# Kernel tuning notes

Measured on AMD Instinct MI355X. Metric: run time of the kernel, lower is better.

The kernel has to match this reference:

```python
import jax, jax.numpy as jnp
import numpy as np

FULL_SCALE = 128.0
R = 0.5
TOPK = 4


def setup_inputs() -> dict:
    key = jax.random.key(0)
    k0, k1, k2, k3, k4 = jax.random.split(key, 5)
    B, Na, Nb, D = 16, 2048, 2048, 512
    coords_a = jax.random.randint(k0, (B, Na, 3), 0, 128, dtype=jnp.int32)
    coords_b = jax.random.randint(k1, (B, Nb, 3), 0, 128, dtype=jnp.int32)
    feats_a = jax.random.normal(k2, (B, Na, D), jnp.float32)
    feats_b = jax.random.normal(k3, (B, Nb, D), jnp.float32)
    W = jax.random.normal(k4, (2 * D, D), jnp.float32) / np.sqrt(2 * D).astype(np.float32)
    bias = jnp.zeros((D,), jnp.float32)
    return {"feats_a": feats_a, "feats_b": feats_b, "W": W, "bias": bias,
            "coords_a": coords_a, "coords_b": coords_b}


def _pairwise_l2(ca, cb):
    # ca: [B,Na,3], cb: [B,Nb,3] -> [B,Na,Nb], scaled by full_scale
    x2 = jnp.sum(ca * ca, axis=-1)[:, :, None]
    y2 = jnp.sum(cb * cb, axis=-1)[:, None, :]
    sq = x2 + y2 - 2.0 * jnp.einsum('bnd,bmd->bnm', ca, cb)
    return jnp.sqrt(jnp.clip(sq, 0.0, None)) / FULL_SCALE


def reference(feats_a, feats_b, W, bias, coords_a, coords_b):
    ca = coords_a.astype(jnp.float32)
    cb = coords_b.astype(jnp.float32)
    dist = _pairwise_l2(ca, cb)                       # [B,Na,Nb]
    neg_top, idx = jax.lax.top_k(-dist, TOPK)         # smallest TOPK distances
    dist_w = R - jnp.clip(-neg_top, 0.0, R)           # [B,Na,k]
    # gather neighbor features: [B,Na,k,D]
    b_f = jnp.take_along_axis(feats_b[:, None, :, :], idx[:, :, :, None], axis=2)
    a_f = feats_a[:, :, None, :]                      # broadcast over k
    h = jnp.concatenate([b_f, a_f - b_f], axis=-1)    # [B,Na,k,2D]
    fused = jnp.sum(jax.nn.relu(h @ W + bias) * dist_w[..., None], axis=2)  # [B,Na,D]
    # ME.cat(a, tmp): concatenate features along channel dim
    return jnp.concatenate([feats_a, fused], axis=-1)  # [B,Na,2D]
```

## Files before the change

kernel.cpp:

```cpp
#include <hip/hip_runtime.h>
#include <hip/hip_bf16.h>
#include <cstdint>
#include <cstddef>

#define NA   2048
#define NB   2048
#define DD   512

typedef __attribute__((ext_vector_type(8))) short bf16x8;
typedef __attribute__((ext_vector_type(4))) float f32x4;
typedef unsigned short u16;
typedef unsigned int   u32;

__device__ __forceinline__ u16 f2b_hw(float f) {
    u32 w;
    asm("v_cvt_pk_bf16_f32 %0, %1, %2" : "=v"(w) : "v"(f), "v"(f));
    return (u16)w;
}
__device__ __forceinline__ float b2f(u16 h) {
    return __uint_as_float(((u32)h) << 16);
}
__device__ __forceinline__ u32 umin32(u32 a, u32 b) { return a < b ? a : b; }
__device__ __forceinline__ u32 umax32(u32 a, u32 b) { return a > b ? a : b; }
__device__ __forceinline__ u32 med3u(u32 a, u32 b, u32 c) {
    return umax32(umin32(a, b), umin32(umax32(a, b), c));
}
__device__ __forceinline__ bf16x8 cvt8(f32x4 v0, f32x4 v1) {
    u32 w0, w1, w2, w3;
    asm("v_cvt_pk_bf16_f32 %0, %1, %2" : "=v"(w0) : "v"(v0[0]), "v"(v0[1]));
    asm("v_cvt_pk_bf16_f32 %0, %1, %2" : "=v"(w1) : "v"(v0[2]), "v"(v0[3]));
    asm("v_cvt_pk_bf16_f32 %0, %1, %2" : "=v"(w2) : "v"(v1[0]), "v"(v1[1]));
    asm("v_cvt_pk_bf16_f32 %0, %1, %2" : "=v"(w3) : "v"(v1[2]), "v"(v1[3]));
    union { u32 u[4]; bf16x8 v; } cv;
    cv.u[0] = w0; cv.u[1] = w1; cv.u[2] = w2; cv.u[3] = w3;
    return cv.v;
}

#define GLDS16(gsrc, ldst)                                                  \
    __builtin_amdgcn_global_load_lds(                                       \
        (const __attribute__((address_space(1))) void*)(gsrc),              \
        (__attribute__((address_space(3))) void*)(ldst), 16, 0, 0)

__global__ __launch_bounds__(256) void prep_w(const float* __restrict__ W,
                                              u16* __restrict__ W2T,
                                              u16* __restrict__ WdT) {
    __shared__ float s2[64][65];
    __shared__ float sd[64][65];
    int kb = blockIdx.x * 64, nb = blockIdx.y * 64;
    int tid = threadIdx.x;
    int c = tid & 63, r0 = tid >> 6;
    #pragma unroll
    for (int p = 0; p < 16; ++p) {
        int r = p * 4 + r0;
        float w1 = W[(size_t)(kb + r) * DD + nb + c];
        float w2 = W[(size_t)(512 + kb + r) * DD + nb + c];
        s2[r][c] = w2;
        sd[r][c] = w1 - w2;
    }
    __syncthreads();
    #pragma unroll
    for (int p = 0; p < 16; ++p) {
        int n = p * 4 + r0;
        W2T[(size_t)(nb + n) * DD + kb + c] = f2b_hw(s2[c][n]);
        WdT[(size_t)(nb + n) * DD + kb + c] = f2b_hw(sd[c][n]);
    }
}

__global__ __launch_bounds__(512) void topk_kernel(const int* __restrict__ ca,
                                                   const int* __restrict__ cb,
                                                   int* __restrict__ idx_out,
                                                   float* __restrict__ w_out) {
    __shared__ u32 pcb[NB];
    __shared__ u32 part[3 * 128 * 4];
    int b = blockIdx.y;
    int tid = threadIdx.x;
    for (int p = tid; p < NB; p += 512) {
        const int* c = cb + ((size_t)b * NB + p) * 3;
        pcb[p] = (u32)c[0] | ((u32)c[1] << 8) | ((u32)c[2] << 16);
    }
    __syncthreads();

    int q = tid & 127, g = tid >> 7;
    int i = blockIdx.x * 128 + q;
    const int* ac = ca + ((size_t)b * NA + i) * 3;
    int ax = ac[0], ay = ac[1], az = ac[2];

    u32 k0 = ~0u, k1 = ~0u, k2 = ~0u, k3 = ~0u;
    int j0 = g * 512;
    #pragma unroll 8
    for (int jj = 0; jj < 512; ++jj) {
        int j = j0 + jj;
        u32 p = pcb[j];
        int dx = ax - (int)(p & 255u);
        int dy = ay - (int)((p >> 8) & 255u);
        int dz = az - (int)(p >> 16);
        u32 s = (u32)(__mul24(dx, dx) + __mul24(dy, dy) + __mul24(dz, dz));
        u32 key = (s << 11) | (u32)j;
        u32 nk0 = umin32(k0, key);
        u32 nk1 = med3u(key, k0, k1);
        u32 nk2 = med3u(key, k1, k2);
        u32 nk3 = med3u(key, k2, k3);
        k0 = nk0; k1 = nk1; k2 = nk2; k3 = nk3;
    }
    if (g) {
        u32* pp = &part[((g - 1) * 128 + q) * 4];
        pp[0] = k0; pp[1] = k1; pp[2] = k2; pp[3] = k3;
    }
    __syncthreads();
    if (g == 0) {
        #pragma unroll
        for (int L = 0; L < 3; ++L) {
            const u32* pp = &part[(L * 128 + q) * 4];
            #pragma unroll
            for (int t = 0; t < 4; ++t) {
                u32 key = pp[t];
                u32 nk0 = umin32(k0, key);
                u32 nk1 = med3u(key, k0, k1);
                u32 nk2 = med3u(key, k1, k2);
                u32 nk3 = med3u(key, k2, k3);
                k0 = nk0; k1 = nk1; k2 = nk2; k3 = nk3;
            }
        }
        size_t o = ((size_t)b * NA + i) * 4;
        u32 ks[4] = {k0, k1, k2, k3};
        #pragma unroll
        for (int t = 0; t < 4; ++t) {
            idx_out[o + t] = (int)(ks[t] & 2047u);
            float d = sqrtf((float)(ks[t] >> 11)) * (1.0f / 128.0f);
            w_out[o + t] = 0.5f - fminf(d, 0.5f);
        }
    }
}

__global__ __launch_bounds__(256, 1) void gemm_qp(
    const float* __restrict__ fa, const float* __restrict__ fb,
    const u16* __restrict__ W2T, const u16* __restrict__ WdT,
    u16* __restrict__ Pb, u16* __restrict__ Qb) {

    __shared__ __align__(16) char smem[65536];

    const int bid  = blockIdx.x;
    const int half = bid >> 9;
    const int idx  = bid & 511;
    const float* A  = half ? fa : fb;
    const u16*   BT = half ? W2T : WdT;
    u16*         C  = half ? Pb : Qb;

    const int tid  = threadIdx.x;
    const int lane = tid & 63;
    const int wave = tid >> 6;
    const int m0   = (idx >> 1) << 7;
    const int n0   = (idx & 1) << 8;
    const int l15  = lane & 15;
    const int fq   = lane >> 4;
    const int wr   = (wave >> 1) << 6;
    const int wc   = (wave & 1) << 7;

    int aflat[4]; const float* asp[4];
    #pragma unroll
    for (int i = 0; i < 4; ++i) {
        int flat = i * 256 + tid;
        int row = flat >> 3, pq = flat & 7;
        aflat[i] = flat;
        asp[i] = A + (size_t)(m0 + row) * DD + ((pq ^ (row & 7)) << 2);
    }
    int bflat[4]; const u16* bsp[4];
    #pragma unroll
    for (int i = 0; i < 4; ++i) {
        int flat = i * 256 + tid;
        int row = flat >> 2, pq = flat & 3;
        bflat[i] = flat;
        bsp[i] = BT + (size_t)(n0 + row) * DD + ((pq ^ ((row >> 1) & 3)) << 3);
    }

    int aoff[4][2], boff[8];
    #pragma unroll
    for (int mf = 0; mf < 4; ++mf) {
        int R = wr + mf * 16 + l15;
        aoff[mf][0] = R * 128 + (((2 * fq) ^ (R & 7)) << 4);
        aoff[mf][1] = R * 128 + (((2 * fq + 1) ^ (R & 7)) << 4);
    }
    #pragma unroll
    for (int nf = 0; nf < 8; ++nf) {
        int R = wc + nf * 16 + l15;
        boff[nf] = 16384 + R * 64 + ((fq ^ ((R >> 1) & 3)) << 4);
    }

    f32x4 acc[4][8];
    #pragma unroll
    for (int mf = 0; mf < 4; ++mf)
        #pragma unroll
        for (int nf = 0; nf < 8; ++nf)
            acc[mf][nf] = (f32x4){0.f, 0.f, 0.f, 0.f};

#define STAGE(kk, bufb)                                                      \
    { _Pragma("unroll") for (int i = 0; i < 4; ++i)                          \
          GLDS16(asp[i] + (kk), smem + (bufb) + aflat[i] * 16);              \
      _Pragma("unroll") for (int i = 0; i < 4; ++i)                          \
          GLDS16(bsp[i] + (kk), smem + (bufb) + 16384 + bflat[i] * 16); }

    STAGE(0, 0);

    #pragma unroll 1
    for (int t = 0; t < 16; ++t) {
        const int cur = (t & 1) * 32768;
        if (t < 15) {
            STAGE((t + 1) * 32, 32768 - cur);
            asm volatile("s_waitcnt vmcnt(8)" ::: "memory");
        } else {
            asm volatile("s_waitcnt vmcnt(0)" ::: "memory");
        }
        __builtin_amdgcn_s_barrier();

        bf16x8 af[4], bfr[8];
        #pragma unroll
        for (int mf = 0; mf < 4; ++mf) {
            f32x4 lo = *(const f32x4*)(smem + cur + aoff[mf][0]);
            f32x4 hi = *(const f32x4*)(smem + cur + aoff[mf][1]);
            af[mf] = cvt8(lo, hi);
        }
        #pragma unroll
        for (int nf = 0; nf < 8; ++nf)
            bfr[nf] = *(const bf16x8*)(smem + cur + boff[nf]);
        #pragma unroll
        for (int mf = 0; mf < 4; ++mf)
            #pragma unroll
            for (int nf = 0; nf < 8; ++nf)
                acc[mf][nf] = __builtin_amdgcn_mfma_f32_16x16x32_bf16(
                    af[mf], bfr[nf], acc[mf][nf], 0, 0, 0);

        __builtin_amdgcn_s_barrier();
    }

    const int r4 = (lane >> 4) * 4;
    #pragma unroll
    for (int mf = 0; mf < 4; ++mf)
        #pragma unroll
        for (int nf = 0; nf < 8; ++nf)
            #pragma unroll
            for (int j = 0; j < 4; ++j) {
                int row = m0 + wr + mf * 16 + r4 + j;
                int col = n0 + wc + nf * 16 + l15;
                C[(size_t)row * DD + col] = f2b_hw(acc[mf][nf][j]);
            }
}

__global__ __launch_bounds__(256) void epilogue_kernel(
    const float* __restrict__ fa, const u16* __restrict__ Pb,
    const u16* __restrict__ Qb, const int* __restrict__ idxb,
    const float* __restrict__ wb, const float* __restrict__ bias,
    float* __restrict__ out) {

    int bid = blockIdx.x;
    int ob  = (bid & 7) * 1024 + (bid >> 3);
    int tid  = threadIdx.x;
    int r    = ob * 4 + (tid >> 6);
    int lane = tid & 63;
    int c8   = lane * 8;
    int b    = r >> 11;

    const int*   ip = idxb + (size_t)r * 4;
    const float* wp = wb + (size_t)r * 4;
    int   i0 = ip[0], i1 = ip[1], i2 = ip[2], i3 = ip[3];
    float w0 = wp[0], w1 = wp[1], w2 = wp[2], w3 = wp[3];

    const float* ar = fa + (size_t)r * DD + c8;
    f32x4 a0 = *(const f32x4*)ar;
    f32x4 a1 = *(const f32x4*)(ar + 4);

    bf16x8 pv = *(const bf16x8*)(Pb + (size_t)r * DD + c8);
    f32x4 bia0 = *(const f32x4*)(bias + c8);
    f32x4 bia1 = *(const f32x4*)(bias + c8 + 4);

    size_t qbase = ((size_t)b << 11) * DD;
    bf16x8 qv0 = *(const bf16x8*)(Qb + qbase + (size_t)i0 * DD + c8);
    bf16x8 qv1 = *(const bf16x8*)(Qb + qbase + (size_t)i1 * DD + c8);
    bf16x8 qv2 = *(const bf16x8*)(Qb + qbase + (size_t)i2 * DD + c8);
    bf16x8 qv3 = *(const bf16x8*)(Qb + qbase + (size_t)i3 * DD + c8);

    float base[8], acc[8];
    #pragma unroll
    for (int j = 0; j < 8; ++j) {
        float bj = (j < 4) ? bia0[j] : bia1[j - 4];
        base[j] = b2f((u16)pv[j]) + bj;
        acc[j] = 0.f;
    }
    #pragma unroll
    for (int j = 0; j < 8; ++j) {
        acc[j] += fmaxf(base[j] + b2f((u16)qv0[j]), 0.f) * w0;
        acc[j] += fmaxf(base[j] + b2f((u16)qv1[j]), 0.f) * w1;
        acc[j] += fmaxf(base[j] + b2f((u16)qv2[j]), 0.f) * w2;
        acc[j] += fmaxf(base[j] + b2f((u16)qv3[j]), 0.f) * w3;
    }

    float* orow = out + (size_t)r * 1024;
    *(f32x4*)(orow + c8)     = a0;
    *(f32x4*)(orow + c8 + 4) = a1;
    f32x4 o0 = {acc[0], acc[1], acc[2], acc[3]};
    f32x4 o1 = {acc[4], acc[5], acc[6], acc[7]};
    *(f32x4*)(orow + 512 + c8)     = o0;
    *(f32x4*)(orow + 512 + c8 + 4) = o1;
}

extern "C" void kernel_launch(void* const* d_in, const int* in_sizes, int n_in,
                              void* d_out, int out_size, void* d_ws, size_t ws_size,
                              hipStream_t stream) {
    const float* fa   = (const float*)d_in[0];
    const float* fb   = (const float*)d_in[1];
    const float* W    = (const float*)d_in[2];
    const float* bias = (const float*)d_in[3];
    const int*   ca   = (const int*)d_in[4];
    const int*   cb   = (const int*)d_in[5];
    float* out = (float*)d_out;

    char* ws = (char*)d_ws;
    u16*   Qb   = (u16*)(ws);
    u16*   Pb   = (u16*)(ws + 33554432);
    u16*   W2T  = (u16*)(ws + 67108864);
    u16*   WdT  = (u16*)(ws + 67633152);
    int*   idxb = (int*)(ws + 68157440);
    float* wb   = (float*)(ws + 68681728);

    dim3 pg(8, 8);
    prep_w<<<pg, 256, 0, stream>>>(W, W2T, WdT);

    dim3 tg(16, 16);
    topk_kernel<<<tg, 512, 0, stream>>>(ca, cb, idxb, wb);

    gemm_qp<<<1024, 256, 0, stream>>>(fa, fb, W2T, WdT, Pb, Qb);

    epilogue_kernel<<<8192, 256, 0, stream>>>(fa, Pb, Qb, idxb, wb, bias, out);
}
```

Before: 148.4 us.

## Convert A tile to bf16 in registers before LDS and fuse feats_a copy into GEMM

```diff
diff --git a/kernel.cpp b/kernel.cpp
--- a/kernel.cpp
+++ b/kernel.cpp
@@ -135,9 +135,10 @@
 __global__ __launch_bounds__(256, 1) void gemm_qp(
     const float* __restrict__ fa, const float* __restrict__ fb,
     const u16* __restrict__ W2T, const u16* __restrict__ WdT,
-    u16* __restrict__ Pb, u16* __restrict__ Qb) {
-
-    __shared__ __align__(16) char smem[65536];
+    u16* __restrict__ Pb, u16* __restrict__ Qb,
+    float* __restrict__ out) {
+
+    __shared__ __align__(16) char smem[49152];
 
     const int bid  = blockIdx.x;
     const int half = bid >> 9;
@@ -145,6 +146,7 @@
     const float* A  = half ? fa : fb;
     const u16*   BT = half ? W2T : WdT;
     u16*         C  = half ? Pb : Qb;
+    const bool doStore = half && !(idx & 1);
 
     const int tid  = threadIdx.x;
     const int lane = tid & 63;
@@ -156,34 +158,37 @@
     const int wr   = (wave >> 1) << 6;
     const int wc   = (wave & 1) << 7;
 
-    int aflat[4]; const float* asp[4];
-    #pragma unroll
-    for (int i = 0; i < 4; ++i) {
+    const float* agp[2];
+    float*       ogp[2];
+    int          awoff[2];
+    #pragma unroll
+    for (int i = 0; i < 2; ++i) {
         int flat = i * 256 + tid;
-        int row = flat >> 3, pq = flat & 7;
-        aflat[i] = flat;
-        asp[i] = A + (size_t)(m0 + row) * DD + ((pq ^ (row & 7)) << 2);
-    }
-    int bflat[4]; const u16* bsp[4];
+        int row = flat >> 2, q = flat & 3;
+        agp[i]  = A + (size_t)(m0 + row) * DD + q * 8;
+        ogp[i]  = out + (size_t)(m0 + row) * 1024 + q * 8;
+        awoff[i] = row * 64 + ((q ^ ((row >> 1) & 3)) << 4);
+    }
+    const u16* bsp[4];
+    int        bdst[4];
     #pragma unroll
     for (int i = 0; i < 4; ++i) {
         int flat = i * 256 + tid;
         int row = flat >> 2, pq = flat & 3;
-        bflat[i] = flat;
-        bsp[i] = BT + (size_t)(n0 + row) * DD + ((pq ^ ((row >> 1) & 3)) << 3);
-    }
-
-    int aoff[4][2], boff[8];
+        bsp[i]  = BT + (size_t)(n0 + row) * DD + ((pq ^ ((row >> 1) & 3)) << 3);
+        bdst[i] = 8192 + flat * 16;
+    }
+
+    int aoff[4], boff[8];
     #pragma unroll
     for (int mf = 0; mf < 4; ++mf) {
         int R = wr + mf * 16 + l15;
-        aoff[mf][0] = R * 128 + (((2 * fq) ^ (R & 7)) << 4);
-        aoff[mf][1] = R * 128 + (((2 * fq + 1) ^ (R & 7)) << 4);
+        aoff[mf] = R * 64 + ((fq ^ ((R >> 1) & 3)) << 4);
     }
     #pragma unroll
     for (int nf = 0; nf < 8; ++nf) {
         int R = wc + nf * 16 + l15;
-        boff[nf] = 16384 + R * 64 + ((fq ^ ((R >> 1) & 3)) << 4);
+        boff[nf] = 8192 + R * 64 + ((fq ^ ((R >> 1) & 3)) << 4);
     }
 
     f32x4 acc[4][8];
@@ -193,43 +198,66 @@
         for (int nf = 0; nf < 8; ++nf)
             acc[mf][nf] = (f32x4){0.f, 0.f, 0.f, 0.f};
 
-#define STAGE(kk, bufb)                                                      \
+    f32x4 ar0a, ar0b, ar1a, ar1b;
+
+#define AISSUE(kk)                                                           \
+    { ar0a = *(const f32x4*)(agp[0] + (kk));                                 \
+      ar0b = *(const f32x4*)(agp[0] + (kk) + 4);                             \
+      ar1a = *(const f32x4*)(agp[1] + (kk));                                 \
+      ar1b = *(const f32x4*)(agp[1] + (kk) + 4);                             \
+      asm volatile("" ::: "memory"); }
+
+#define BISSUE(kk, bufb)                                                     \
     { _Pragma("unroll") for (int i = 0; i < 4; ++i)                          \
-          GLDS16(asp[i] + (kk), smem + (bufb) + aflat[i] * 16);              \
-      _Pragma("unroll") for (int i = 0; i < 4; ++i)                          \
-          GLDS16(bsp[i] + (kk), smem + (bufb) + 16384 + bflat[i] * 16); }
-
-    STAGE(0, 0);
+          GLDS16(bsp[i] + (kk), smem + (bufb) + bdst[i]); }
+
+#define AWRITE(bufb)                                                         \
+    { *(bf16x8*)(smem + (bufb) + awoff[0]) = cvt8(ar0a, ar0b);               \
+      *(bf16x8*)(smem + (bufb) + awoff[1]) = cvt8(ar1a, ar1b); }
+
+#define ASTORE(kk)                                                           \
+    { *(f32x4*)(ogp[0] + (kk))     = ar0a;                                   \
+      *(f32x4*)(ogp[0] + (kk) + 4) = ar0b;                                   \
+      *(f32x4*)(ogp[1] + (kk))     = ar1a;                                   \
+      *(f32x4*)(ogp[1] + (kk) + 4) = ar1b; }
+
+#define COMPUTE(bufb)                                                        \
+    { bf16x8 af[4], bfr[8];                                                  \
+      _Pragma("unroll") for (int mf = 0; mf < 4; ++mf)                       \
+          af[mf] = *(const bf16x8*)(smem + (bufb) + aoff[mf]);               \
+      _Pragma("unroll") for (int nf = 0; nf < 8; ++nf)                       \
+          bfr[nf] = *(const bf16x8*)(smem + (bufb) + boff[nf]);              \
+      _Pragma("unroll") for (int mf = 0; mf < 4; ++mf)                       \
+          _Pragma("unroll") for (int nf = 0; nf < 8; ++nf)                   \
+              acc[mf][nf] = __builtin_amdgcn_mfma_f32_16x16x32_bf16(         \
+                  af[mf], bfr[nf], acc[mf][nf], 0, 0, 0); }
+
+#define TAIL(kk, bufb)                                                       \
+    { asm volatile("s_waitcnt vmcnt(4)" ::: "memory");     \
+      AWRITE(bufb);                                                          \
+      if (doStore) {                                                         \
+          ASTORE(kk);                                                        \
+          asm volatile("s_waitcnt vmcnt(4)" ::: "memory");       \
+      } else {                                                               \
+          asm volatile("s_waitcnt vmcnt(0)" ::: "memory");       \
+      }                                                                      \
+      asm volatile("s_waitcnt lgkmcnt(0)" ::: "memory");                     \
+      __builtin_amdgcn_s_barrier(); }
+
+    AISSUE(0);
+    BISSUE(0, 0);
+    TAIL(0, 0);
 
     #pragma unroll 1
     for (int t = 0; t < 16; ++t) {
-        const int cur = (t & 1) * 32768;
+        const int cur = (t & 1) * 24576;
+        const int nxt = 24576 - cur;
         if (t < 15) {
-            STAGE((t + 1) * 32, 32768 - cur);
-            asm volatile("s_waitcnt vmcnt(8)" ::: "memory");
-        } else {
-            asm volatile("s_waitcnt vmcnt(0)" ::: "memory");
+            AISSUE((t + 1) * 32);
+            BISSUE((t + 1) * 32, nxt);
         }
-        __builtin_amdgcn_s_barrier();
-
-        bf16x8 af[4], bfr[8];
-        #pragma unroll
-        for (int mf = 0; mf < 4; ++mf) {
-            f32x4 lo = *(const f32x4*)(smem + cur + aoff[mf][0]);
-            f32x4 hi = *(const f32x4*)(smem + cur + aoff[mf][1]);
-            af[mf] = cvt8(lo, hi);
-        }
-        #pragma unroll
-        for (int nf = 0; nf < 8; ++nf)
-            bfr[nf] = *(const bf16x8*)(smem + cur + boff[nf]);
-        #pragma unroll
-        for (int mf = 0; mf < 4; ++mf)
-            #pragma unroll
-            for (int nf = 0; nf < 8; ++nf)
-                acc[mf][nf] = __builtin_amdgcn_mfma_f32_16x16x32_bf16(
-                    af[mf], bfr[nf], acc[mf][nf], 0, 0, 0);
-
-        __builtin_amdgcn_s_barrier();
+        COMPUTE(cur);
+        if (t < 15) TAIL((t + 1) * 32, nxt);
     }
 
     const int r4 = (lane >> 4) * 4;
@@ -246,10 +274,9 @@
 }
 
 __global__ __launch_bounds__(256) void epilogue_kernel(
-    const float* __restrict__ fa, const u16* __restrict__ Pb,
-    const u16* __restrict__ Qb, const int* __restrict__ idxb,
-    const float* __restrict__ wb, const float* __restrict__ bias,
-    float* __restrict__ out) {
+    const u16* __restrict__ Pb, const u16* __restrict__ Qb,
+    const int* __restrict__ idxb, const float* __restrict__ wb,
+    const float* __restrict__ bias, float* __restrict__ out) {
 
     int bid = blockIdx.x;
     int ob  = (bid & 7) * 1024 + (bid >> 3);
@@ -264,10 +291,6 @@
     int   i0 = ip[0], i1 = ip[1], i2 = ip[2], i3 = ip[3];
     float w0 = wp[0], w1 = wp[1], w2 = wp[2], w3 = wp[3];
 
-    const float* ar = fa + (size_t)r * DD + c8;
-    f32x4 a0 = *(const f32x4*)ar;
-    f32x4 a1 = *(const f32x4*)(ar + 4);
-
     bf16x8 pv = *(const bf16x8*)(Pb + (size_t)r * DD + c8);
     f32x4 bia0 = *(const f32x4*)(bias + c8);
     f32x4 bia1 = *(const f32x4*)(bias + c8 + 4);
@@ -293,13 +316,11 @@
         acc[j] += fmaxf(base[j] + b2f((u16)qv3[j]), 0.f) * w3;
     }
 
-    float* orow = out + (size_t)r * 1024;
-    *(f32x4*)(orow + c8)     = a0;
-    *(f32x4*)(orow + c8 + 4) = a1;
+    float* orow = out + (size_t)r * 1024 + 512;
     f32x4 o0 = {acc[0], acc[1], acc[2], acc[3]};
     f32x4 o1 = {acc[4], acc[5], acc[6], acc[7]};
-    *(f32x4*)(orow + 512 + c8)     = o0;
-    *(f32x4*)(orow + 512 + c8 + 4) = o1;
+    *(f32x4*)(orow + c8)     = o0;
+    *(f32x4*)(orow + c8 + 4) = o1;
 }
 
 extern "C" void kernel_launch(void* const* d_in, const int* in_sizes, int n_in,
@@ -327,7 +348,7 @@
     dim3 tg(16, 16);
     topk_kernel<<<tg, 512, 0, stream>>>(ca, cb, idxb, wb);
 
-    gemm_qp<<<1024, 256, 0, stream>>>(fa, fb, W2T, WdT, Pb, Qb);
-
-    epilogue_kernel<<<8192, 256, 0, stream>>>(fa, Pb, Qb, idxb, wb, bias, out);
-}
+    gemm_qp<<<1024, 256, 0, stream>>>(fa, fb, W2T, WdT, Pb, Qb, out);
+
+    epilogue_kernel<<<8192, 256, 0, stream>>>(Pb, Qb, idxb, wb, bias, out);
+}
```

Result: slower. 166.6 us (+12.3%).
